# Kernel tuning notes

Measured on AMD Instinct MI355X. Metric: run time of the kernel, lower is better.

The kernel has to match this reference:

```python
import jax, jax.numpy as jnp
import numpy as np

B, Q, N, E, D, H, EDIM = 64, 50, 32, 64, 128, 4, 8
NEG = -1e30

def _ln(x, g, b, eps=1e-5):
    mu = x.mean(-1, keepdims=True)
    var = ((x - mu) ** 2).mean(-1, keepdims=True)
    return (x - mu) / jnp.sqrt(var + eps) * g + b

def setup_inputs():
    key = jax.random.key(0)
    ks = jax.random.split(key, 12)
    s = 1.0 / np.sqrt(D)
    return {
        "query_embeddings": jax.random.normal(ks[0], (B, Q, N, D), jnp.float32),
        "query_maskings": jnp.ones((B, Q, N), jnp.int32),
        "edge_indexes": jax.random.randint(ks[1], (B, Q, 2, E), 0, N, dtype=jnp.int32),
        "edge_weights": jax.random.randint(ks[2], (B, Q, E), 0, 2, dtype=jnp.int32),
        "edge_maskings": jnp.ones((B, Q, E), jnp.int32),
        "ln1_g": jnp.ones((D,), jnp.float32),
        "ln1_b": jnp.zeros((D,), jnp.float32),
        "emb_table": jax.random.normal(ks[3], (2, EDIM), jnp.float32),
        "Wl": jax.random.normal(ks[4], (D, H * D), jnp.float32) * s,
        "bl": jnp.zeros((H * D,), jnp.float32),
        "Wr": jax.random.normal(ks[5], (D, H * D), jnp.float32) * s,
        "br": jnp.zeros((H * D,), jnp.float32),
        "We": jax.random.normal(ks[6], (EDIM, H * D), jnp.float32) / np.sqrt(EDIM),
        "att": jax.random.normal(ks[7], (H, D), jnp.float32) * s,
        "gat_b": jnp.zeros((D,), jnp.float32),
        "W1": jax.random.normal(ks[8], (D, D), jnp.float32) * s,
        "b1": jnp.zeros((D,), jnp.float32),
        "W2": jax.random.normal(ks[9], (D, D), jnp.float32) * s,
        "b2": jnp.zeros((D,), jnp.float32),
        "ln2_g": jnp.ones((D,), jnp.float32),
        "ln2_b": jnp.zeros((D,), jnp.float32),
    }

def _gat_graph(x, src, dst, eemb, emask, Wl, bl, Wr, br, We, att, gat_b):
    # GATv2Conv, heads=H, concat=False, add_self_loops=True (fill_value='mean')
    # x [N,D]; src,dst [E]; eemb [E,EDIM]; emask [E] float
    xl = (x @ Wl + bl).reshape(N, H, D)
    xr = (x @ Wr + br).reshape(N, H, D)
    # self-loop edge_attr = mean of incoming (valid) edge attrs per target node
    ecnt = jax.ops.segment_sum(emask, dst, num_segments=N)
    loop_attr = jax.ops.segment_sum(eemb * emask[:, None], dst, num_segments=N) / jnp.maximum(ecnt, 1.0)[:, None]
    e = (eemb @ We).reshape(E, H, D)
    le = (loop_attr @ We).reshape(N, H, D)
    z = jax.nn.leaky_relu(xl[src] + xr[dst] + e, 0.2)
    logits = jnp.where(emask[:, None] > 0, jnp.einsum('ehd,hd->eh', z, att), NEG)
    zs = jax.nn.leaky_relu(xl + xr + le, 0.2)  # self-loop terms
    logits_s = jnp.einsum('nhd,hd->nh', zs, att)
    # segment softmax over incoming edges + self loop
    m = jnp.maximum(jax.ops.segment_max(logits, dst, num_segments=N), logits_s)  # [N,H]
    exp_e = jnp.where(emask[:, None] > 0, jnp.exp(logits - m[dst]), 0.0)
    exp_s = jnp.exp(logits_s - m)
    denom = jax.ops.segment_sum(exp_e, dst, num_segments=N) + exp_s
    agg = jax.ops.segment_sum(xl[src] * (exp_e / denom[dst])[:, :, None], dst, num_segments=N)
    agg = agg + xl * (exp_s / denom)[:, :, None]
    return agg.mean(axis=1) + gat_b  # concat=False -> mean over heads, + bias

def _forward(query_embeddings, ln1_g, ln1_b, emb_table, Wl, bl, Wr, br, We, att, gat_b,
             W1, b1, W2, b2, ln2_g, ln2_b,
             query_maskings, edge_indexes, edge_weights, edge_maskings):
    x = _ln(query_embeddings, ln1_g, ln1_b)                 # [B,Q,N,D]
    nmask = query_maskings.astype(jnp.float32)              # [B,Q,N]
    emask = edge_maskings.astype(jnp.float32)               # [B,Q,E]
    valid = ((query_maskings.sum(-1) > 0) & (edge_maskings.sum(-1) > 0)).astype(jnp.float32)  # [B,Q]
    eemb = emb_table[edge_weights]                          # [B,Q,E,EDIM]
    G = B * Q
    xf = x.reshape(G, N, D)
    srcf = edge_indexes[:, :, 0, :].reshape(G, E)
    dstf = edge_indexes[:, :, 1, :].reshape(G, E)
    eembf = eemb.reshape(G, E, EDIM)
    emaskf = emask.reshape(G, E)
    gat = jax.vmap(_gat_graph, in_axes=(0, 0, 0, 0, 0) + (None,) * 7)
    gout = gat(xf, srcf, dstf, eembf, emaskf, Wl, bl, Wr, br, We, att, gat_b)  # [G,N,D]
    h = jax.nn.leaky_relu(gout @ W1 + b1, 0.01) @ W2 + b2   # FFN (dropout = eval no-op)
    nmf = nmask.reshape(G, N)
    pooled = (h * nmf[:, :, None]).sum(1) / jnp.maximum(nmf.sum(1), 1.0)[:, None]  # global mean pool
    res = pooled.reshape(B, Q, D) * valid[:, :, None]       # invalid queries stay zero
    return _ln(res, ln2_g, ln2_b)

def reference(query_embeddings, query_maskings, edge_indexes, edge_weights, edge_maskings,
              ln1_g, ln1_b, emb_table, Wl, bl, Wr, br, We, att, gat_b,
              W1, b1, W2, b2, ln2_g, ln2_b):
    return _forward(query_embeddings, ln1_g, ln1_b, emb_table, Wl, bl, Wr, br, We, att, gat_b,
                    W1, b1, W2, b2, ln2_g, ln2_b,
                    query_maskings, edge_indexes, edge_weights, edge_maskings)
```

## Files before the change

### kernel.cpp

```cpp
#include <hip/hip_runtime.h>
#include <math.h>

#define B_ 64
#define Q_ 50
#define N_ 32
#define E_ 64
#define D_ 128
#define H_ 4
#define EDIM_ 8
#define G_ (B_*Q_)

#define WLP_OFF 0
#define WRP_OFF 131072
#define W1P_OFF 262144
#define W2P_OFF 294912
#define EW_OFF  327680

typedef __attribute__((ext_vector_type(8))) short short8;
typedef __attribute__((ext_vector_type(4))) float f32x4;
typedef __attribute__((ext_vector_type(4))) unsigned uint4e;
typedef __attribute__((ext_vector_type(2))) unsigned uint2e;
typedef __attribute__((ext_vector_type(2))) _Float16 half2e;
typedef __attribute__((ext_vector_type(2))) __fp16 fp16v2;
typedef unsigned short ushort_t;
typedef unsigned long long u64;

__device__ __forceinline__ int boff(int r, int d) {
  return (r << 7) + ((d & 0x78) ^ ((r & 15) << 3)) + (d & 7);
}

__device__ __forceinline__ ushort_t f2b(float f) {
  unsigned u = __float_as_uint(f);
  u += 0x7fffu + ((u >> 16) & 1u);
  return (ushort_t)(u >> 16);
}
__device__ __forceinline__ float b2f(ushort_t u) {
  return __uint_as_float(((unsigned)u) << 16);
}
__device__ __forceinline__ unsigned cvtpk(float lo, float hi) {
  unsigned r;
  asm("v_cvt_pk_bf16_f32 %0, %1, %2" : "=v"(r) : "v"(lo), "v"(hi));
  return r;
}
__device__ __forceinline__ unsigned pkrtz(float lo, float hi) {
  union { fp16v2 h; unsigned u; } x;
  x.h = __builtin_amdgcn_cvt_pkrtz(lo, hi);
  return x.u;
}
__device__ __forceinline__ half2e u2h(unsigned u) {
  union { unsigned u; half2e h; } x; x.u = u; return x.h;
}
__device__ __forceinline__ float leakyf(float v, float s) {
  return fmaxf(v, s * v);
}
__device__ __forceinline__ void syncb() {
  asm volatile("s_waitcnt lgkmcnt(0)" ::: "memory");
  __builtin_amdgcn_s_barrier();
  asm volatile("" ::: "memory");
}

__global__ __launch_bounds__(256)
void pack_weights(const float* __restrict__ Wl, const float* __restrict__ Wr,
                  const float* __restrict__ W1, const float* __restrict__ W2,
                  const float* __restrict__ embT, const float* __restrict__ We,
                  unsigned char* __restrict__ ws)
{
  const int i = blockIdx.x * 256 + threadIdx.x;
  ushort_t* wlp = (ushort_t*)(ws + WLP_OFF);
  ushort_t* wrp = (ushort_t*)(ws + WRP_OFF);
  ushort_t* w1p = (ushort_t*)(ws + W1P_OFF);
  ushort_t* w2p = (ushort_t*)(ws + W2P_OFF);
  float* ew = (float*)(ws + EW_OFF);
  if (i < 65536) {
    const int kk = i & 31, n = (i >> 5) & 127, q = (i >> 12) & 3, h = i >> 14;
    wlp[i] = f2b(Wl[(q * 32 + kk) * (H_ * D_) + h * D_ + n]);
    wrp[i] = f2b(Wr[(q * 32 + kk) * (H_ * D_) + h * D_ + n]);
  } else if (i < 65536 + 16384) {
    const int j = i - 65536;
    const int kk = j & 31, n = (j >> 5) & 127, q = j >> 12;
    w1p[j] = f2b(W1[(q * 32 + kk) * D_ + n]);
    w2p[j] = f2b(W2[(q * 32 + kk) * D_ + n]);
  } else if (i < 65536 + 16384 + 1024) {
    const int j = i - 65536 - 16384;
    const int w = j >> 9, hd = j & 511;
    float a = 0.f;
#pragma unroll
    for (int k = 0; k < EDIM_; ++k) a = fmaf(embT[w * EDIM_ + k], We[k * (H_ * D_) + hd], a);
    ew[j] = a;
  }
}

template <bool F16OUT, bool LEAKY>
__device__ __forceinline__ void gemm_e(const short8 aF[2][4], const ushort_t* __restrict__ Bp,
                                       const float* __restrict__ bias, float slope,
                                       ushort_t* __restrict__ dst, int lane, int nq)
{
#pragma unroll
  for (int nt = 0; nt < 2; ++nt) {
    const int colw = nq * 32 + nt * 16 + (lane & 15);
    const int oc0 = nq * 32 + nt * 16 + ((lane >> 4) << 2);
    const float4 bb = *(const float4*)&bias[oc0];
    f32x4 acc0 = {0.f, 0.f, 0.f, 0.f}, acc1 = {0.f, 0.f, 0.f, 0.f};
#pragma unroll
    for (int q = 0; q < 4; ++q) {
      const short8 b = *(const short8*)&Bp[((q << 7) + colw) * 32 + ((lane >> 4) << 3)];
      acc0 = __builtin_amdgcn_mfma_f32_16x16x32_bf16(b, aF[0][q], acc0, 0, 0, 0);
      acc1 = __builtin_amdgcn_mfma_f32_16x16x32_bf16(b, aF[1][q], acc1, 0, 0, 0);
    }
#pragma unroll
    for (int cc = 0; cc < 2; ++cc) {
      const f32x4 a = cc ? acc1 : acc0;
      const int node = cc * 16 + (lane & 15);
      float v0 = a[0] + bb.x, v1 = a[1] + bb.y, v2 = a[2] + bb.z, v3 = a[3] + bb.w;
      if (LEAKY) {
        v0 = leakyf(v0, slope); v1 = leakyf(v1, slope);
        v2 = leakyf(v2, slope); v3 = leakyf(v3, slope);
      }
      uint2e o;
      if (F16OUT) {
        o.x = pkrtz(v0, v1);
        o.y = pkrtz(v2, v3);
      } else {
        o.x = cvtpk(v0, v1);
        o.y = cvtpk(v2, v3);
      }
      *(uint2e*)&dst[boff(node, oc0)] = o;
    }
  }
}

__global__ __launch_bounds__(256, 10)
void gat_main(const unsigned char* __restrict__ ws,
              const float* __restrict__ qe,
              const float* __restrict__ ln1g, const float* __restrict__ ln1b,
              const int* __restrict__ qmask, const int* __restrict__ eidx,
              const int* __restrict__ ewt, const int* __restrict__ emsk,
              const float* __restrict__ bl, const float* __restrict__ br,
              const float* __restrict__ att, const float* __restrict__ gatb,
              const float* __restrict__ b1, const float* __restrict__ b2,
              const float* __restrict__ ln2g, const float* __restrict__ ln2b,
              float* __restrict__ out)
{
  const int g = blockIdx.x, t = threadIdx.x;
  const int lane = t & 63, wave = t >> 6;

  __shared__ __align__(16) ushort_t sX[N_ * D_];
  __shared__ __align__(16) ushort_t sXl[N_ * D_];
  __shared__ __align__(16) ushort_t sXr[N_ * D_];
  __shared__ u64 sInc[N_];
  __shared__ int sSrc[E_], sDst[E_], sWt[E_];
  __shared__ float sEm[E_], sNm[N_], sC0[N_], sC1[N_];
  __shared__ float sValid, sNmSum;

  ushort_t* sEW  = sX;
  ushort_t* sAtt = sX + 1024;
  float* sExpE = (float*)(sX + 1536);
  float* sExpS = (float*)(sX + 1664);
  float* sPool = (float*)(sX + 1728);

  const ushort_t* wlp = (const ushort_t*)(ws + WLP_OFF);
  const ushort_t* wrp = (const ushort_t*)(ws + WRP_OFF);
  const ushort_t* w1p = (const ushort_t*)(ws + W1P_OFF);
  const ushort_t* w2p = (const ushort_t*)(ws + W2P_OFF);

  {
    const int r = t >> 3, d0 = (t & 7) << 4;
    const f32x4* src4 = (const f32x4*)(qe + ((size_t)g * N_ + r) * D_ + d0);
    f32x4 v4[4];
#pragma unroll
    for (int p = 0; p < 4; ++p) v4[p] = __builtin_nontemporal_load(src4 + p);
    const float* v = (const float*)v4;
    float s = 0.f, ss = 0.f;
#pragma unroll
    for (int i = 0; i < 16; ++i) { float x = v[i]; s += x; ss += x * x; }
#pragma unroll
    for (int m = 1; m < 8; m <<= 1) { s += __shfl_xor(s, m); ss += __shfl_xor(ss, m); }
    const float mu = s * (1.f / 128.f);
    const float inv = rsqrtf(ss * (1.f / 128.f) - mu * mu + 1e-5f);
    const f32x4* gg = (const f32x4*)&ln1g[d0];
    const f32x4* bb = (const f32x4*)&ln1b[d0];
    float o[16];
#pragma unroll
    for (int p = 0; p < 4; ++p) {
      const f32x4 g4 = gg[p], b4 = bb[p];
#pragma unroll
      for (int k = 0; k < 4; ++k)
        o[p * 4 + k] = (v[p * 4 + k] - mu) * inv * g4[k] + b4[k];
    }
    uint4e w0, w1;
    w0.x = cvtpk(o[0], o[1]);  w0.y = cvtpk(o[2], o[3]);
    w0.z = cvtpk(o[4], o[5]);  w0.w = cvtpk(o[6], o[7]);
    w1.x = cvtpk(o[8], o[9]);  w1.y = cvtpk(o[10], o[11]);
    w1.z = cvtpk(o[12], o[13]); w1.w = cvtpk(o[14], o[15]);
    *(uint4e*)&sX[boff(r, d0)] = w0;
    *(uint4e*)&sX[boff(r, d0 + 8)] = w1;
  }
  if (t < E_) {
    sSrc[t] = eidx[(size_t)g * 2 * E_ + t];
    sDst[t] = eidx[(size_t)g * 2 * E_ + E_ + t];
    sWt[t] = ewt[(size_t)g * E_ + t];
    sEm[t] = (float)emsk[(size_t)g * E_ + t];
  } else if (t < 96) {
    sNm[t - 64] = (float)qmask[(size_t)g * N_ + (t - 64)];
  }
  syncb();

  short8 aF[2][4];
#pragma unroll
  for (int c = 0; c < 2; ++c)
#pragma unroll
    for (int q = 0; q < 4; ++q)
      aF[c][q] = *(const short8*)&sX[boff(c * 16 + (lane & 15), q * 32 + ((lane >> 4) << 3))];

  {
    const int dl = sDst[lane];
    const float eml = sEm[lane];
    const int wtl = sWt[lane];
    const bool val = eml > 0.f;
    const u64 wt0m = __ballot(wtl == 0);
#pragma unroll
    for (int k = 0; k < 8; ++k) {
      const int n = wave * 8 + k;
      const u64 inc = __ballot(val && dl == n);
      if (lane == k) {
        sInc[n] = inc;
        const float cnt = (float)__popcll(inc);
        const float c0 = (float)__popcll(inc & wt0m);
        const float rinv = 1.f / fmaxf(cnt, 1.f);
        sC0[n] = c0 * rinv;
        sC1[n] = (cnt - c0) * rinv;
      }
    }
    if (wave == 3) {
      float nmv = (lane < 32) ? sNm[lane] : 0.f;
      float emv = eml;
#pragma unroll
      for (int m = 1; m < 64; m <<= 1) { nmv += __shfl_xor(nmv, m); emv += __shfl_xor(emv, m); }
      if (lane == 0) {
        sNmSum = nmv;
        sValid = (nmv > 0.f && emv > 0.f) ? 1.f : 0.f;
      }
    }
  }
  syncb();

  {
    const float* ewg = (const float*)(ws + EW_OFF);
    const f32x4 e4 = *(const f32x4*)&ewg[t << 2];
    uint2e p;
    p.x = pkrtz(e4[0], e4[1]);
    p.y = pkrtz(e4[2], e4[3]);
    *(uint2e*)&sEW[t << 2] = p;
    if (t < 128) {
      const f32x4 a4 = *(const f32x4*)&att[t << 2];
      uint2e q;
      q.x = pkrtz(a4[0], a4[1]);
      q.y = pkrtz(a4[2], a4[3]);
      *(uint2e*)&sAtt[t << 2] = q;
    }
  }

  const half2e pslope = {(_Float16)0.2f, (_Float16)0.2f};
  half2e accA[4] = {}, accB[4] = {};

  for (int h = 0; h < H_; ++h) {
    gemm_e<true, false>(aF, wlp + h * 16384, bl + h * D_, 0.f, sXl, lane, wave);
    gemm_e<true, false>(aF, wrp + h * 16384, br + h * D_, 0.f, sXr, lane, wave);
    syncb();
    {
      const int e = t >> 2, qu = t & 3;
      const int sn = sSrc[e], dn = sDst[e];
      const int ewb = (sWt[e] << 9) + (h << 7);
      float dx = 0.f, dy = 0.f;
#pragma unroll
      for (int ch = 0; ch < 4; ++ch) {
        const int dd = qu * 32 + ch * 8;
        const uint4e xlu = *(const uint4e*)&sXl[boff(sn, dd)];
        const uint4e xru = *(const uint4e*)&sXr[boff(dn, dd)];
        const uint4e ewu = *(const uint4e*)&sEW[ewb + dd];
        const uint4e atu = *(const uint4e*)&sAtt[(h << 7) + dd];
#pragma unroll
        for (int k = 0; k < 4; ++k) {
          half2e z = u2h(xlu[k]) + u2h(xru[k]) + u2h(ewu[k]);
          z = __builtin_elementwise_max(z, z * pslope);
          if (k & 1) dy = __builtin_amdgcn_fdot2(z, u2h(atu[k]), dy, false);
          else       dx = __builtin_amdgcn_fdot2(z, u2h(atu[k]), dx, false);
        }
      }
      float dot = dx + dy;
      dot += __shfl_xor(dot, 1);
      dot += __shfl_xor(dot, 2);
      const float ex = (sEm[e] > 0.f) ? __expf(dot) : 0.f;
      if (qu == 0) sExpE[e] = ex;
    }
    {
      const int n = t >> 3, l8 = t & 7;
      const half2e c02 = {(_Float16)sC0[n], (_Float16)sC0[n]};
      const half2e c12 = {(_Float16)sC1[n], (_Float16)sC1[n]};
      float dx = 0.f, dy = 0.f;
#pragma unroll
      for (int ch = 0; ch < 2; ++ch) {
        const int dd = (l8 << 4) + ch * 8;
        const uint4e xlu = *(const uint4e*)&sXl[boff(n, dd)];
        const uint4e xru = *(const uint4e*)&sXr[boff(n, dd)];
        const uint4e e0u = *(const uint4e*)&sEW[(h << 7) + dd];
        const uint4e e1u = *(const uint4e*)&sEW[512 + (h << 7) + dd];
        const uint4e atu = *(const uint4e*)&sAtt[(h << 7) + dd];
#pragma unroll
        for (int k = 0; k < 4; ++k) {
          half2e lw = u2h(e0u[k]) * c02 + u2h(e1u[k]) * c12;
          half2e z = u2h(xlu[k]) + u2h(xru[k]) + lw;
          z = __builtin_elementwise_max(z, z * pslope);
          if (k & 1) dy = __builtin_amdgcn_fdot2(z, u2h(atu[k]), dy, false);
          else       dx = __builtin_amdgcn_fdot2(z, u2h(atu[k]), dx, false);
        }
      }
      float dot = dx + dy;
      dot += __shfl_xor(dot, 1);
      dot += __shfl_xor(dot, 2);
      dot += __shfl_xor(dot, 4);
      if (l8 == 0) sExpS[n] = __expf(dot);
    }
    syncb();
    {
      const int n = t >> 3, l8 = t & 7, db = l8 << 4;
      const float es = sExpS[n];
      const u64 mb = sInc[n];
      float den = es;
      u64 m2 = mb;
      while (m2) { const int e = __builtin_ctzll(m2); m2 &= m2 - 1; den += sExpE[e]; }
      const float rd = 0.25f / den;
      m2 = mb;
      while (m2) {
        const int e = __builtin_ctzll(m2); m2 &= m2 - 1;
        const _Float16 wh = (_Float16)(rd * sExpE[e]);
        const half2e w2 = {wh, wh};
        const int sn = sSrc[e];
        const uint4e a0 = *(const uint4e*)&sXl[boff(sn, db)];
        const uint4e a1 = *(const uint4e*)&sXl[boff(sn, db + 8)];
#pragma unroll
        for (int k = 0; k < 4; ++k) {
          accA[k] = u2h(a0[k]) * w2 + accA[k];
          accB[k] = u2h(a1[k]) * w2 + accB[k];
        }
      }
      const _Float16 wsh = (_Float16)(rd * es);
      const half2e ws2 = {wsh, wsh};
      const uint4e s0 = *(const uint4e*)&sXl[boff(n, db)];
      const uint4e s1 = *(const uint4e*)&sXl[boff(n, db + 8)];
#pragma unroll
      for (int k = 0; k < 4; ++k) {
        accA[k] = u2h(s0[k]) * ws2 + accA[k];
        accB[k] = u2h(s1[k]) * ws2 + accB[k];
      }
    }
    syncb();
  }

  {
    const int n = t >> 3, l8 = t & 7, db = l8 << 4;
    const float4 g0 = *(const float4*)&gatb[db];
    const float4 g1 = *(const float4*)&gatb[db + 4];
    const float4 g2 = *(const float4*)&gatb[db + 8];
    const float4 g3 = *(const float4*)&gatb[db + 12];
    const float gv[16] = {g0.x, g0.y, g0.z, g0.w, g1.x, g1.y, g1.z, g1.w,
                          g2.x, g2.y, g2.z, g2.w, g3.x, g3.y, g3.z, g3.w};
    uint4e o0, o1;
    unsigned* po0 = (unsigned*)&o0;
    unsigned* po1 = (unsigned*)&o1;
#pragma unroll
    for (int k = 0; k < 4; ++k) {
      po0[k] = cvtpk((float)accA[k].x + gv[2 * k], (float)accA[k].y + gv[2 * k + 1]);
      po1[k] = cvtpk((float)accB[k].x + gv[8 + 2 * k], (float)accB[k].y + gv[8 + 2 * k + 1]);
    }
    *(uint4e*)&sX[boff(n, db)] = o0;
    *(uint4e*)&sX[boff(n, db + 8)] = o1;
  }
  syncb();

  {
    short8 aG[2][4];
#pragma unroll
    for (int c = 0; c < 2; ++c)
#pragma unroll
      for (int q = 0; q < 4; ++q)
        aG[c][q] = *(const short8*)&sX[boff(c * 16 + (lane & 15), q * 32 + ((lane >> 4) << 3))];
    gemm_e<false, true>(aG, w1p, b1, 0.01f, sXl, lane, wave);
    syncb();
#pragma unroll
    for (int c = 0; c < 2; ++c)
#pragma unroll
      for (int q = 0; q < 4; ++q)
        aG[c][q] = *(const short8*)&sXl[boff(c * 16 + (lane & 15), q * 32 + ((lane >> 4) << 3))];
    gemm_e<false, false>(aG, w2p, b2, 0.f, sXr, lane, wave);
  }
  syncb();

  if (t < D_) {
    float acc = 0.f;
    for (int n = 0; n < N_; ++n) acc = fmaf(b2f(sXr[boff(n, t)]), sNm[n], acc);
    sPool[t] = acc * (1.f / fmaxf(sNmSum, 1.f)) * sValid;
  }
  syncb();
  if (t < 64) {
    const float v0 = sPool[t], v1 = sPool[t + 64];
    float s = v0 + v1, ss = v0 * v0 + v1 * v1;
#pragma unroll
    for (int m = 1; m < 64; m <<= 1) { s += __shfl_xor(s, m); ss += __shfl_xor(ss, m); }
    const float mu = s * (1.f / 128.f);
    const float inv = rsqrtf(ss * (1.f / 128.f) - mu * mu + 1e-5f);
    float* op = out + (size_t)g * D_;
    __builtin_nontemporal_store((v0 - mu) * inv * ln2g[t] + ln2b[t], op + t);
    __builtin_nontemporal_store((v1 - mu) * inv * ln2g[t + 64] + ln2b[t + 64], op + t + 64);
  }
}

extern "C" void kernel_launch(void* const* d_in, const int* in_sizes, int n_in,
                              void* d_out, int out_size, void* d_ws, size_t ws_size,
                              hipStream_t stream) {
  (void)in_sizes; (void)n_in; (void)out_size; (void)ws_size;
  const float* qe   = (const float*)d_in[0];
  const int*   qm   = (const int*)d_in[1];
  const int*   ei   = (const int*)d_in[2];
  const int*   ew   = (const int*)d_in[3];
  const int*   em   = (const int*)d_in[4];
  const float* ln1g = (const float*)d_in[5];
  const float* ln1b = (const float*)d_in[6];
  const float* embT = (const float*)d_in[7];
  const float* Wl   = (const float*)d_in[8];
  const float* bl   = (const float*)d_in[9];
  const float* Wr   = (const float*)d_in[10];
  const float* br   = (const float*)d_in[11];
  const float* We   = (const float*)d_in[12];
  const float* att  = (const float*)d_in[13];
  const float* gatb = (const float*)d_in[14];
  const float* W1   = (const float*)d_in[15];
  const float* b1   = (const float*)d_in[16];
  const float* W2   = (const float*)d_in[17];
  const float* b2   = (const float*)d_in[18];
  const float* ln2g = (const float*)d_in[19];
  const float* ln2b = (const float*)d_in[20];
  float* out = (float*)d_out;
  unsigned char* ws = (unsigned char*)d_ws;

  pack_weights<<<dim3(324), dim3(256), 0, stream>>>(Wl, Wr, W1, W2, embT, We, ws);
  gat_main<<<dim3(G_), dim3(256), 0, stream>>>(ws, qe, ln1g, ln1b, qm, ei, ew, em,
                                               bl, br, att, gatb, b1, b2, ln2g, ln2b, out);
}
```

Baseline: 134.5 us.

## Compute all heads' projections up front and batch per-head attention phases

Instead of looping over heads with projection GEMMs, edge scoring, self-loop scoring and aggregation separated by barriers per head, the kernel now computes all four heads' Wl/Wr projections into a larger shared buffer (64KB of bf16 tiles). It then runs the edge and node scoring for all heads in a single pass and aggregates across heads in one pass. This cuts the number of block barriers and gives more independent work per phase for latency hiding. In exchange, LDS use grows about 3x and the launch-bounds occupancy hint drops from 10 to 4 blocks per CU, which may reduce latency hiding across blocks.

```diff
diff --git a/kernel.cpp b/kernel.cpp
--- a/kernel.cpp
+++ b/kernel.cpp
@@ -129,7 +129,7 @@
   }
 }
 
-__global__ __launch_bounds__(256, 10)
+__global__ __launch_bounds__(256, 4)
 void gat_main(const unsigned char* __restrict__ ws,
               const float* __restrict__ qe,
               const float* __restrict__ ln1g, const float* __restrict__ ln1b,
@@ -144,19 +144,17 @@
   const int g = blockIdx.x, t = threadIdx.x;
   const int lane = t & 63, wave = t >> 6;
 
-  __shared__ __align__(16) ushort_t sX[N_ * D_];
-  __shared__ __align__(16) ushort_t sXl[N_ * D_];
-  __shared__ __align__(16) ushort_t sXr[N_ * D_];
+  __shared__ __align__(16) ushort_t sT[8 * N_ * D_];
+  __shared__ __align__(16) ushort_t sEW[1024];
+  __shared__ __align__(16) ushort_t sAtt[512];
+  __shared__ float sExpE[H_][E_];
+  __shared__ float sExpS[H_][N_];
+  __shared__ float sPool[D_];
   __shared__ u64 sInc[N_];
   __shared__ int sSrc[E_], sDst[E_], sWt[E_];
   __shared__ float sEm[E_], sNm[N_], sC0[N_], sC1[N_];
   __shared__ float sValid, sNmSum;
-
-  ushort_t* sEW  = sX;
-  ushort_t* sAtt = sX + 1024;
-  float* sExpE = (float*)(sX + 1536);
-  float* sExpS = (float*)(sX + 1664);
-  float* sPool = (float*)(sX + 1728);
+#define T(i) (sT + (i) * (N_ * D_))
 
   const ushort_t* wlp = (const ushort_t*)(ws + WLP_OFF);
   const ushort_t* wrp = (const ushort_t*)(ws + WRP_OFF);
@@ -192,58 +190,9 @@
     w0.z = cvtpk(o[4], o[5]);  w0.w = cvtpk(o[6], o[7]);
     w1.x = cvtpk(o[8], o[9]);  w1.y = cvtpk(o[10], o[11]);
     w1.z = cvtpk(o[12], o[13]); w1.w = cvtpk(o[14], o[15]);
-    *(uint4e*)&sX[boff(r, d0)] = w0;
-    *(uint4e*)&sX[boff(r, d0 + 8)] = w1;
-  }
-  if (t < E_) {
-    sSrc[t] = eidx[(size_t)g * 2 * E_ + t];
-    sDst[t] = eidx[(size_t)g * 2 * E_ + E_ + t];
-    sWt[t] = ewt[(size_t)g * E_ + t];
-    sEm[t] = (float)emsk[(size_t)g * E_ + t];
-  } else if (t < 96) {
-    sNm[t - 64] = (float)qmask[(size_t)g * N_ + (t - 64)];
-  }
-  syncb();
-
-  short8 aF[2][4];
-#pragma unroll
-  for (int c = 0; c < 2; ++c)
-#pragma unroll
-    for (int q = 0; q < 4; ++q)
-      aF[c][q] = *(const short8*)&sX[boff(c * 16 + (lane & 15), q * 32 + ((lane >> 4) << 3))];
-
-  {
-    const int dl = sDst[lane];
-    const float eml = sEm[lane];
-    const int wtl = sWt[lane];
-    const bool val = eml > 0.f;
-    const u64 wt0m = __ballot(wtl == 0);
-#pragma unroll
-    for (int k = 0; k < 8; ++k) {
-      const int n = wave * 8 + k;
-      const u64 inc = __ballot(val && dl == n);
-      if (lane == k) {
-        sInc[n] = inc;
-        const float cnt = (float)__popcll(inc);
-        const float c0 = (float)__popcll(inc & wt0m);
-        const float rinv = 1.f / fmaxf(cnt, 1.f);
-        sC0[n] = c0 * rinv;
-        sC1[n] = (cnt - c0) * rinv;
-      }
-    }
-    if (wave == 3) {
-      float nmv = (lane < 32) ? sNm[lane] : 0.f;
-      float emv = eml;
-#pragma unroll
-      for (int m = 1; m < 64; m <<= 1) { nmv += __shfl_xor(nmv, m); emv += __shfl_xor(emv, m); }
-      if (lane == 0) {
-        sNmSum = nmv;
-        sValid = (nmv > 0.f && emv > 0.f) ? 1.f : 0.f;
-      }
-    }
-  }
-  syncb();
-
+    *(uint4e*)&T(0)[boff(r, d0)] = w0;
+    *(uint4e*)&T(0)[boff(r, d0 + 8)] = w1;
+  }
   {
     const float* ewg = (const float*)(ws + EW_OFF);
     const f32x4 e4 = *(const f32x4*)&ewg[t << 2];
@@ -259,50 +208,109 @@
       *(uint2e*)&sAtt[t << 2] = q;
     }
   }
+  if (t < E_) {
+    sSrc[t] = eidx[(size_t)g * 2 * E_ + t];
+    sDst[t] = eidx[(size_t)g * 2 * E_ + E_ + t];
+    sWt[t] = ewt[(size_t)g * E_ + t];
+    sEm[t] = (float)emsk[(size_t)g * E_ + t];
+  } else if (t < 96) {
+    sNm[t - 64] = (float)qmask[(size_t)g * N_ + (t - 64)];
+  }
+  syncb();
+
+  short8 aF[2][4];
+#pragma unroll
+  for (int c = 0; c < 2; ++c)
+#pragma unroll
+    for (int q = 0; q < 4; ++q)
+      aF[c][q] = *(const short8*)&T(0)[boff(c * 16 + (lane & 15), q * 32 + ((lane >> 4) << 3))];
+  {
+    const int dl = sDst[lane];
+    const float eml = sEm[lane];
+    const int wtl = sWt[lane];
+    const bool val = eml > 0.f;
+    const u64 wt0m = __ballot(wtl == 0);
+#pragma unroll
+    for (int k = 0; k < 8; ++k) {
+      const int n = wave * 8 + k;
+      const u64 inc = __ballot(val && dl == n);
+      if (lane == k) {
+        sInc[n] = inc;
+        const float cnt = (float)__popcll(inc);
+        const float c0 = (float)__popcll(inc & wt0m);
+        const float rinv = 1.f / fmaxf(cnt, 1.f);
+        sC0[n] = c0 * rinv;
+        sC1[n] = (cnt - c0) * rinv;
+      }
+    }
+    if (wave == 3) {
+      float nmv = (lane < 32) ? sNm[lane] : 0.f;
+      float emv = eml;
+#pragma unroll
+      for (int m = 1; m < 64; m <<= 1) { nmv += __shfl_xor(nmv, m); emv += __shfl_xor(emv, m); }
+      if (lane == 0) {
+        sNmSum = nmv;
+        sValid = (nmv > 0.f && emv > 0.f) ? 1.f : 0.f;
+      }
+    }
+  }
+  syncb();
+
+#pragma unroll
+  for (int h = 0; h < H_; ++h) {
+    gemm_e<true, false>(aF, wlp + h * 16384, bl + h * D_, 0.f, T(h), lane, wave);
+    gemm_e<true, false>(aF, wrp + h * 16384, br + h * D_, 0.f, T(4 + h), lane, wave);
+  }
+  syncb();
 
   const half2e pslope = {(_Float16)0.2f, (_Float16)0.2f};
-  half2e accA[4] = {}, accB[4] = {};
-
-  for (int h = 0; h < H_; ++h) {
-    gemm_e<true, false>(aF, wlp + h * 16384, bl + h * D_, 0.f, sXl, lane, wave);
-    gemm_e<true, false>(aF, wrp + h * 16384, br + h * D_, 0.f, sXr, lane, wave);
-    syncb();
-    {
-      const int e = t >> 2, qu = t & 3;
-      const int sn = sSrc[e], dn = sDst[e];
-      const int ewb = (sWt[e] << 9) + (h << 7);
-      float dx = 0.f, dy = 0.f;
-#pragma unroll
-      for (int ch = 0; ch < 4; ++ch) {
-        const int dd = qu * 32 + ch * 8;
-        const uint4e xlu = *(const uint4e*)&sXl[boff(sn, dd)];
-        const uint4e xru = *(const uint4e*)&sXr[boff(dn, dd)];
-        const uint4e ewu = *(const uint4e*)&sEW[ewb + dd];
+
+  {
+    const int e = t >> 2, qu = t & 3;
+    const int sn = sSrc[e], dn = sDst[e];
+    const int wb = sWt[e] << 9;
+    float dx[H_] = {}, dy[H_] = {};
+#pragma unroll
+    for (int ch = 0; ch < 4; ++ch) {
+      const int dd = qu * 32 + ch * 8;
+      const int osn = boff(sn, dd), odn = boff(dn, dd);
+#pragma unroll
+      for (int h = 0; h < H_; ++h) {
+        const uint4e xlu = *(const uint4e*)&T(h)[osn];
+        const uint4e xru = *(const uint4e*)&T(4 + h)[odn];
+        const uint4e ewu = *(const uint4e*)&sEW[wb + (h << 7) + dd];
         const uint4e atu = *(const uint4e*)&sAtt[(h << 7) + dd];
 #pragma unroll
         for (int k = 0; k < 4; ++k) {
           half2e z = u2h(xlu[k]) + u2h(xru[k]) + u2h(ewu[k]);
           z = __builtin_elementwise_max(z, z * pslope);
-          if (k & 1) dy = __builtin_amdgcn_fdot2(z, u2h(atu[k]), dy, false);
-          else       dx = __builtin_amdgcn_fdot2(z, u2h(atu[k]), dx, false);
+          if (k & 1) dy[h] = __builtin_amdgcn_fdot2(z, u2h(atu[k]), dy[h], false);
+          else       dx[h] = __builtin_amdgcn_fdot2(z, u2h(atu[k]), dx[h], false);
         }
       }
-      float dot = dx + dy;
+    }
+    const bool ve = sEm[e] > 0.f;
+#pragma unroll
+    for (int h = 0; h < H_; ++h) {
+      float dot = dx[h] + dy[h];
       dot += __shfl_xor(dot, 1);
       dot += __shfl_xor(dot, 2);
-      const float ex = (sEm[e] > 0.f) ? __expf(dot) : 0.f;
-      if (qu == 0) sExpE[e] = ex;
-    }
-    {
-      const int n = t >> 3, l8 = t & 7;
-      const half2e c02 = {(_Float16)sC0[n], (_Float16)sC0[n]};
-      const half2e c12 = {(_Float16)sC1[n], (_Float16)sC1[n]};
-      float dx = 0.f, dy = 0.f;
-#pragma unroll
-      for (int ch = 0; ch < 2; ++ch) {
-        const int dd = (l8 << 4) + ch * 8;
-        const uint4e xlu = *(const uint4e*)&sXl[boff(n, dd)];
-        const uint4e xru = *(const uint4e*)&sXr[boff(n, dd)];
+      if (qu == 0) sExpE[h][e] = ve ? __expf(dot) : 0.f;
+    }
+  }
+  {
+    const int n = t >> 3, l8 = t & 7;
+    const half2e c02 = {(_Float16)sC0[n], (_Float16)sC0[n]};
+    const half2e c12 = {(_Float16)sC1[n], (_Float16)sC1[n]};
+    float dx[H_] = {}, dy[H_] = {};
+#pragma unroll
+    for (int ch = 0; ch < 2; ++ch) {
+      const int dd = (l8 << 4) + ch * 8;
+      const int on = boff(n, dd);
+#pragma unroll
+      for (int h = 0; h < H_; ++h) {
+        const uint4e xlu = *(const uint4e*)&T(h)[on];
+        const uint4e xru = *(const uint4e*)&T(4 + h)[on];
         const uint4e e0u = *(const uint4e*)&sEW[(h << 7) + dd];
         const uint4e e1u = *(const uint4e*)&sEW[512 + (h << 7) + dd];
         const uint4e atu = *(const uint4e*)&sAtt[(h << 7) + dd];
@@ -311,51 +319,71 @@
           half2e lw = u2h(e0u[k]) * c02 + u2h(e1u[k]) * c12;
           half2e z = u2h(xlu[k]) + u2h(xru[k]) + lw;
           z = __builtin_elementwise_max(z, z * pslope);
-          if (k & 1) dy = __builtin_amdgcn_fdot2(z, u2h(atu[k]), dy, false);
-          else       dx = __builtin_amdgcn_fdot2(z, u2h(atu[k]), dx, false);
+          if (k & 1) dy[h] = __builtin_amdgcn_fdot2(z, u2h(atu[k]), dy[h], false);
+          else       dx[h] = __builtin_amdgcn_fdot2(z, u2h(atu[k]), dx[h], false);
         }
       }
-      float dot = dx + dy;
+    }
+#pragma unroll
+    for (int h = 0; h < H_; ++h) {
+      float dot = dx[h] + dy[h];
       dot += __shfl_xor(dot, 1);
       dot += __shfl_xor(dot, 2);
       dot += __shfl_xor(dot, 4);
-      if (l8 == 0) sExpS[n] = __expf(dot);
-    }
-    syncb();
-    {
-      const int n = t >> 3, l8 = t & 7, db = l8 << 4;
-      const float es = sExpS[n];
-      const u64 mb = sInc[n];
-      float den = es;
-      u64 m2 = mb;
-      while (m2) { const int e = __builtin_ctzll(m2); m2 &= m2 - 1; den += sExpE[e]; }
-      const float rd = 0.25f / den;
-      m2 = mb;
-      while (m2) {
-        const int e = __builtin_ctzll(m2); m2 &= m2 - 1;
-        const _Float16 wh = (_Float16)(rd * sExpE[e]);
+      if (l8 == 0) sExpS[h][n] = __expf(dot);
+    }
+  }
+  syncb();
+
+  half2e accA[4] = {}, accB[4] = {};
+  {
+    const int n = t >> 3, l8 = t & 7, db = l8 << 4;
+    const u64 mb = sInc[n];
+    float den[H_];
+#pragma unroll
+    for (int h = 0; h < H_; ++h) den[h] = sExpS[h][n];
+    u64 m2 = mb;
+    while (m2) {
+      const int e = __builtin_ctzll(m2); m2 &= m2 - 1;
+#pragma unroll
+      for (int h = 0; h < H_; ++h) den[h] += sExpE[h][e];
+    }
+    float rd[H_];
+#pragma unroll
+    for (int h = 0; h < H_; ++h) rd[h] = 0.25f / den[h];
+    m2 = mb;
+    while (m2) {
+      const int e = __builtin_ctzll(m2); m2 &= m2 - 1;
+      const int sn = sSrc[e];
+      const int o0 = boff(sn, db), o1 = boff(sn, db + 8);
+#pragma unroll
+      for (int h = 0; h < H_; ++h) {
+        const _Float16 wh = (_Float16)(rd[h] * sExpE[h][e]);
         const half2e w2 = {wh, wh};
-        const int sn = sSrc[e];
-        const uint4e a0 = *(const uint4e*)&sXl[boff(sn, db)];
-        const uint4e a1 = *(const uint4e*)&sXl[boff(sn, db + 8)];
+        const uint4e a0 = *(const uint4e*)&T(h)[o0];
+        const uint4e a1 = *(const uint4e*)&T(h)[o1];
 #pragma unroll
         for (int k = 0; k < 4; ++k) {
           accA[k] = u2h(a0[k]) * w2 + accA[k];
           accB[k] = u2h(a1[k]) * w2 + accB[k];
         }
       }
-      const _Float16 wsh = (_Float16)(rd * es);
+    }
+    const int o0 = boff(n, db), o1 = boff(n, db + 8);
+#pragma unroll
+    for (int h = 0; h < H_; ++h) {
+      const _Float16 wsh = (_Float16)(rd[h] * sExpS[h][n]);
       const half2e ws2 = {wsh, wsh};
-      const uint4e s0 = *(const uint4e*)&sXl[boff(n, db)];
-      const uint4e s1 = *(const uint4e*)&sXl[boff(n, db + 8)];
+      const uint4e s0 = *(const uint4e*)&T(h)[o0];
+      const uint4e s1 = *(const uint4e*)&T(h)[o1];
 #pragma unroll
       for (int k = 0; k < 4; ++k) {
         accA[k] = u2h(s0[k]) * ws2 + accA[k];
         accB[k] = u2h(s1[k]) * ws2 + accB[k];
       }
     }
-    syncb();
-  }
+  }
+  syncb();
 
   {
     const int n = t >> 3, l8 = t & 7, db = l8 << 4;
@@ -373,8 +401,8 @@
       po0[k] = cvtpk((float)accA[k].x + gv[2 * k], (float)accA[k].y + gv[2 * k + 1]);
       po1[k] = cvtpk((float)accB[k].x + gv[8 + 2 * k], (float)accB[k].y + gv[8 + 2 * k + 1]);
     }
-    *(uint4e*)&sX[boff(n, db)] = o0;
-    *(uint4e*)&sX[boff(n, db + 8)] = o1;
+    *(uint4e*)&T(0)[boff(n, db)] = o0;
+    *(uint4e*)&T(0)[boff(n, db + 8)] = o1;
   }
   syncb();
 
@@ -384,21 +412,21 @@
     for (int c = 0; c < 2; ++c)
 #pragma unroll
       for (int q = 0; q < 4; ++q)
-        aG[c][q] = *(const short8*)&sX[boff(c * 16 + (lane & 15), q * 32 + ((lane >> 4) << 3))];
-    gemm_e<false, true>(aG, w1p, b1, 0.01f, sXl, lane, wave);
+        aG[c][q] = *(const short8*)&T(0)[boff(c * 16 + (lane & 15), q * 32 + ((lane >> 4) << 3))];
+    gemm_e<false, true>(aG, w1p, b1, 0.01f, T(4), lane, wave);
     syncb();
 #pragma unroll
     for (int c = 0; c < 2; ++c)
 #pragma unroll
       for (int q = 0; q < 4; ++q)
-        aG[c][q] = *(const short8*)&sXl[boff(c * 16 + (lane & 15), q * 32 + ((lane >> 4) << 3))];
-    gemm_e<false, false>(aG, w2p, b2, 0.f, sXr, lane, wave);
+        aG[c][q] = *(const short8*)&T(4)[boff(c * 16 + (lane & 15), q * 32 + ((lane >> 4) << 3))];
+    gemm_e<false, false>(aG, w2p, b2, 0.f, T(1), lane, wave);
   }
   syncb();
 
   if (t < D_) {
     float acc = 0.f;
-    for (int n = 0; n < N_; ++n) acc = fmaf(b2f(sXr[boff(n, t)]), sNm[n], acc);
+    for (int n = 0; n < N_; ++n) acc = fmaf(b2f(T(1)[boff(n, t)]), sNm[n], acc);
     sPool[t] = acc * (1.f / fmaxf(sNmSum, 1.f)) * sValid;
   }
   syncb();
@@ -413,6 +441,7 @@
     __builtin_nontemporal_store((v0 - mu) * inv * ln2g[t] + ln2b[t], op + t);
     __builtin_nontemporal_store((v1 - mu) * inv * ln2g[t + 64] + ln2b[t + 64], op + t + 64);
   }
+#undef T
 }
 
 extern "C" void kernel_launch(void* const* d_in, const int* in_sizes, int n_in,
```

Measured after the change: 137.3 us. 1.02x slower.
